# Kernel optimization log

Measured on AMD Instinct MI355X. Metric: run time of the kernel, lower is better.

Reference implementation:

```python
import jax, jax.numpy as jnp
import numpy as np

N, F, D, E, L, T = 20000, 512, 256, 200000, 3, 2  # nodes, raw feat, hidden, edges/etype, layers, etypes


def _layernorm(x, g, b, eps=1e-5):
    mu = jnp.mean(x, axis=-1, keepdims=True)
    var = jnp.mean(jnp.square(x - mu), axis=-1, keepdims=True)
    return (x - mu) * jax.lax.rsqrt(var + eps) * g + b


def setup_inputs() -> dict:
    key = jax.random.key(0)
    ks = jax.random.split(key, 12)
    s = 0.02
    return {
        "x": jax.random.normal(ks[0], (N, F), dtype=jnp.float32),
        "src": jax.random.randint(ks[1], (T, E), 0, N, dtype=jnp.int32),
        "dst": jax.random.randint(ks[2], (T, E), 0, N, dtype=jnp.int32),
        # HeteroLinear (single ntype)
        "Wlin": jax.random.normal(ks[3], (D, F), dtype=jnp.float32) * s,
        "blin": jnp.zeros((D,), dtype=jnp.float32),
        # stacked per-layer, per-etype SAGEConv('pool') params
        "Wpool": jax.random.normal(ks[4], (L, T, D, D), dtype=jnp.float32) * s,
        "bpool": jnp.zeros((L, T, D), dtype=jnp.float32),
        "Wself": jax.random.normal(ks[5], (L, T, D, D), dtype=jnp.float32) * s,
        "Wneigh": jax.random.normal(ks[6], (L, T, D, D), dtype=jnp.float32) * s,
        "bconv": jnp.zeros((L, T, D), dtype=jnp.float32),
        "gamma": jnp.ones((L, T, D), dtype=jnp.float32),
        "beta": jnp.zeros((L, T, D), dtype=jnp.float32),
    }


def reference(x, src, dst, Wlin, blin, Wpool, bpool, Wself, Wneigh, bconv, gamma, beta):
    n = x.shape[0]
    # HeteroLinear: raw features -> embed
    h = x @ Wlin.T + blin
    for l in range(L):
        out = None
        for t in range(T):  # per edge-type SAGEConv, aggregator='pool'
            hp = jax.nn.relu(h @ Wpool[l, t].T + bpool[l, t])        # fc_pool + relu on src nodes
            m = hp[src[t]]                                            # gather [E, D]
            neigh = jax.ops.segment_max(m, dst[t], num_segments=n)    # max-pool reduce
            neigh = jnp.where(jnp.isneginf(neigh), 0.0, neigh)        # zero-in-degree -> 0 (DGL)
            rst = h @ Wself[l, t].T + neigh @ Wneigh[l, t].T + bconv[l, t]
            if l < L - 1:
                rst = jax.nn.relu(rst)                                # activation before norm
            rst = _layernorm(rst, gamma[l, t], beta[l, t])
            out = rst if out is None else out + rst                   # HeteroGraphConv 'sum'
        h = out
    return h
```

## Files before the change

### kernel.cpp

```cpp
#include <hip/hip_runtime.h>

#define N_NODES 20000
#define F_IN    512
#define D_H     256
#define E_EDGES 200000
#define L_LAYERS 3
#define T_ETYPES 2

typedef __attribute__((ext_vector_type(8))) short bf16x8;
typedef __attribute__((ext_vector_type(4))) float f32x4;

__device__ __forceinline__ unsigned short f2b(float f) {
    unsigned int u = __float_as_uint(f);
    u = (u + 0x7FFFu + ((u >> 16) & 1u)) >> 16;
    return (unsigned short)u;
}
__device__ __forceinline__ unsigned int pack2(float a, float b) {
    return (unsigned int)f2b(a) | ((unsigned int)f2b(b) << 16);
}

__device__ __forceinline__ void gload16(const unsigned short* g, unsigned short* l)
{
    __builtin_amdgcn_global_load_lds(
        (const __attribute__((address_space(1))) void*)g,
        (__attribute__((address_space(3))) void*)l, 16, 0, 0);
}

__device__ __forceinline__ void shuf_one(const float* s, unsigned short* d,
                                         int NO, int K, int i)
{
    const int matsz = NO * K;
    const int mat = i / matsz;
    const int rem = i - mat * matsz;
    const int n = rem / K;
    const int k = rem - n * K;
    const int dst = mat * matsz + ((n >> 7) * (K >> 5) + (k >> 5)) * 4096
                  + (((n >> 4) & 7) << 9) + (((k >> 3) & 3) << 7)
                  + ((n & 15) << 3) + (k & 7);
    d[dst] = f2b(s[i]);
}

__global__ __launch_bounds__(256) void shufw_kernel(
    const float* __restrict__ s0, unsigned short* __restrict__ d0, int NO0, int K0, int n0,
    const float* __restrict__ s1, unsigned short* __restrict__ d1, int NO1, int K1, int n1,
    const float* __restrict__ s2, unsigned short* __restrict__ d2, int NO2, int K2, int n2,
    const float* __restrict__ s3, unsigned short* __restrict__ d3, int NO3, int K3, int n3)
{
    int i = blockIdx.x * 256 + threadIdx.x;
    if (i < n0) { shuf_one(s0, d0, NO0, K0, i); return; }
    if ((i -= n0) < n1) { shuf_one(s1, d1, NO1, K1, i); return; }
    if ((i -= n1) < n2) { shuf_one(s2, d2, NO2, K2, i); return; }
    if ((i -= n2) < n3) { shuf_one(s3, d3, NO3, K3, i); return; }
}

__global__ __launch_bounds__(256) void cvt_bf16_kernel(
    const float* __restrict__ in, unsigned short* __restrict__ out, int n8)
{
    const int i = blockIdx.x * 256 + threadIdx.x;
    if (i < n8) {
        const float4 a = ((const float4*)in)[i * 2];
        const float4 b = ((const float4*)in)[i * 2 + 1];
        uint4 u;
        u.x = pack2(a.x, a.y); u.y = pack2(a.z, a.w);
        u.z = pack2(b.x, b.y); u.w = pack2(b.z, b.w);
        ((uint4*)out)[i] = u;
    }
}

template <int NSTEPS>
__global__ __launch_bounds__(256) void gemm_lds(
    const unsigned short* __restrict__ A,
    const unsigned short* __restrict__ Wf,
    const float* __restrict__ bias, unsigned short* __restrict__ Cout,
    int M, int ldc, int relu)
{
    __shared__ __align__(16) unsigned short As[2][4096];
    __shared__ __align__(16) unsigned short Bs[2][4096];
    const int K = NSTEPS * 32;
    const int tid = threadIdx.x, lane = tid & 63, w = tid >> 6;
    const int wm = w >> 1, wn = w & 1;
    const int bm = blockIdx.y * 128, bn = blockIdx.x * 128;
    const unsigned short* slab0 = Wf + (((size_t)blockIdx.x * NSTEPS) << 12);

    size_t aoff[2];
#pragma unroll
    for (int q = 0; q < 2; ++q) {
        const int c = q * 256 + tid;
        const int mi = c >> 6, ww = c & 63, r = ww & 15, kq = ww >> 4;
        const int rg = min(bm + mi * 16 + r, M - 1);
        aoff[q] = (size_t)rg * K + kq * 8;
    }

    f32x4 acc[4][4] = {};

#define GL_STAGE(S, BUF) do { \
    _Pragma("unroll") \
    for (int q_ = 0; q_ < 2; ++q_) { \
        gload16(A + aoff[q_] + (S) * 32, &As[BUF][(q_ * 256 + w * 64) * 8]); \
        gload16(slab0 + (((size_t)(S)) << 12) + (size_t)(q_ * 256 + tid) * 8, \
                &Bs[BUF][(q_ * 256 + w * 64) * 8]); \
    } \
} while (0)

    GL_STAGE(0, 0);
#pragma unroll
    for (int s = 0; s < NSTEPS; ++s) {
        __syncthreads();
        if (s + 1 < NSTEPS) GL_STAGE(s + 1, (s + 1) & 1);
        const int buf = s & 1;
        bf16x8 a[4], b[4];
#pragma unroll
        for (int mi = 0; mi < 4; ++mi)
            a[mi] = *(const bf16x8*)((const char*)As[buf] + ((wm * 4 + mi) << 10) + lane * 16);
#pragma unroll
        for (int j = 0; j < 4; ++j)
            b[j] = *(const bf16x8*)((const char*)Bs[buf] + ((wn * 4 + j) << 10) + lane * 16);
#pragma unroll
        for (int mi = 0; mi < 4; ++mi)
#pragma unroll
            for (int j = 0; j < 4; ++j)
                acc[mi][j] = __builtin_amdgcn_mfma_f32_16x16x32_bf16(a[mi], b[j], acc[mi][j], 0, 0, 0);
    }
#undef GL_STAGE

    const int cbase = bn + wn * 64 + (lane & 15);
    const int rb = bm + wm * 64 + ((lane >> 4) << 2);
#pragma unroll
    for (int j = 0; j < 4; ++j) {
        const float bj = bias[cbase + j * 16];
#pragma unroll
        for (int mi = 0; mi < 4; ++mi)
#pragma unroll
            for (int r = 0; r < 4; ++r) {
                const int row = rb + mi * 16 + r;
                if (row < M) {
                    float v = acc[mi][j][r] + bj;
                    if (relu) v = fmaxf(v, 0.f);
                    Cout[(size_t)row * ldc + cbase + j * 16] = f2b(v);
                }
            }
    }
}

template <int RELU>
__global__ __launch_bounds__(256) void tail_gemm(
    const unsigned short* __restrict__ h,
    const unsigned short* __restrict__ neigh,
    const unsigned short* __restrict__ Ws,
    const unsigned short* __restrict__ Wn,
    const float* __restrict__ bias,
    float* __restrict__ R)
{
    __shared__ __align__(16) unsigned short As[2][4096];
    __shared__ __align__(16) unsigned short Bs[2][4096];
    const int tid = threadIdx.x, lane = tid & 63, w = tid >> 6;
    const int wm = w >> 1, wn = w & 1;
    const int bm = blockIdx.y * 128;
    const int cs = blockIdx.x;
    const int e  = cs >> 1;
    const unsigned short* Bself  = Ws + (size_t)e * 65536 + (cs & 1) * 32768;
    const unsigned short* Bneigh = Wn + (size_t)e * 65536 + (cs & 1) * 32768;

    size_t aoffH[2], aoffN[2];
#pragma unroll
    for (int q = 0; q < 2; ++q) {
        const int c = q * 256 + tid;
        const int mi = c >> 6, ww = c & 63, r = ww & 15, kq = ww >> 4;
        const int rg = min(bm + mi * 16 + r, N_NODES - 1);
        aoffH[q] = (size_t)rg * 256 + kq * 8;
        aoffN[q] = (size_t)rg * 512 + e * 256 + kq * 8;
    }

    f32x4 acc[4][4] = {};

#define TG_STAGE(S, BUF) do { \
    _Pragma("unroll") \
    for (int q_ = 0; q_ < 2; ++q_) { \
        const unsigned short* as_ = ((S) < 8) ? (h + aoffH[q_] + (S) * 32) \
                                              : (neigh + aoffN[q_] + ((S) - 8) * 32); \
        gload16(as_, &As[BUF][(q_ * 256 + w * 64) * 8]); \
        const unsigned short* bs_ = (((S) < 8) ? (Bself + (S) * 4096) \
                                               : (Bneigh + ((S) - 8) * 4096)) \
                                    + (size_t)(q_ * 256 + tid) * 8; \
        gload16(bs_, &Bs[BUF][(q_ * 256 + w * 64) * 8]); \
    } \
} while (0)

    TG_STAGE(0, 0);
#pragma unroll
    for (int s = 0; s < 16; ++s) {
        __syncthreads();
        if (s + 1 < 16) TG_STAGE(s + 1, (s + 1) & 1);
        const int buf = s & 1;
        bf16x8 a[4], b[4];
#pragma unroll
        for (int mi = 0; mi < 4; ++mi)
            a[mi] = *(const bf16x8*)((const char*)As[buf] + ((wm * 4 + mi) << 10) + lane * 16);
#pragma unroll
        for (int j = 0; j < 4; ++j)
            b[j] = *(const bf16x8*)((const char*)Bs[buf] + ((wn * 4 + j) << 10) + lane * 16);
#pragma unroll
        for (int mi = 0; mi < 4; ++mi)
#pragma unroll
            for (int j = 0; j < 4; ++j)
                acc[mi][j] = __builtin_amdgcn_mfma_f32_16x16x32_bf16(a[mi], b[j], acc[mi][j], 0, 0, 0);
    }
#undef TG_STAGE

    const int cbase = cs * 128 + wn * 64 + (lane & 15);
    const int rb = bm + wm * 64 + ((lane >> 4) << 2);
#pragma unroll
    for (int j = 0; j < 4; ++j) {
        const float bj = bias[cbase + j * 16];
#pragma unroll
        for (int mi = 0; mi < 4; ++mi)
#pragma unroll
            for (int r = 0; r < 4; ++r) {
                const int row = rb + mi * 16 + r;
                if (row < N_NODES) {
                    float v = acc[mi][j][r] + bj;
                    if (RELU) v = fmaxf(v, 0.f);
                    R[(size_t)row * 512 + cbase + j * 16] = v;
                }
            }
    }
}

template <int LAST>
__global__ __launch_bounds__(256) void ln_sum_kernel(
    const float* __restrict__ R,
    const float* __restrict__ gamma,
    const float* __restrict__ beta,
    void* __restrict__ outp)
{
    const int row  = blockIdx.x * 4 + (threadIdx.x >> 6);
    const int lane = threadIdx.x & 63;
    const float4 v0 = ((const float4*)R)[(size_t)row * 128 + lane];
    const float4 v1 = ((const float4*)R)[(size_t)row * 128 + 64 + lane];
    float s0 = v0.x + v0.y + v0.z + v0.w;
    float q0 = v0.x * v0.x + v0.y * v0.y + v0.z * v0.z + v0.w * v0.w;
    float s1 = v1.x + v1.y + v1.z + v1.w;
    float q1 = v1.x * v1.x + v1.y * v1.y + v1.z * v1.z + v1.w * v1.w;
#pragma unroll
    for (int o = 1; o < 64; o <<= 1) {
        s0 += __shfl_xor(s0, o); q0 += __shfl_xor(q0, o);
        s1 += __shfl_xor(s1, o); q1 += __shfl_xor(q1, o);
    }
    const float m0 = s0 * (1.f / 256.f), m1 = s1 * (1.f / 256.f);
    const float i0 = rsqrtf(q0 * (1.f / 256.f) - m0 * m0 + 1e-5f);
    const float i1 = rsqrtf(q1 * (1.f / 256.f) - m1 * m1 + 1e-5f);
    const float4 g0 = ((const float4*)gamma)[lane];
    const float4 b0 = ((const float4*)beta)[lane];
    const float4 g1 = ((const float4*)(gamma + 256))[lane];
    const float4 b1 = ((const float4*)(beta + 256))[lane];
    const float o0 = (v0.x - m0) * i0 * g0.x + b0.x + (v1.x - m1) * i1 * g1.x + b1.x;
    const float o1 = (v0.y - m0) * i0 * g0.y + b0.y + (v1.y - m1) * i1 * g1.y + b1.y;
    const float o2 = (v0.z - m0) * i0 * g0.z + b0.z + (v1.z - m1) * i1 * g1.z + b1.z;
    const float o3 = (v0.w - m0) * i0 * g0.w + b0.w + (v1.w - m1) * i1 * g1.w + b1.w;
    if (LAST) {
        ((float4*)outp)[(size_t)row * 64 + lane] = make_float4(o0, o1, o2, o3);
    } else {
        ushort4 u;
        u.x = f2b(o0); u.y = f2b(o1); u.z = f2b(o2); u.w = f2b(o3);
        ((ushort4*)outp)[(size_t)row * 64 + lane] = u;
    }
}

__global__ __launch_bounds__(256) void count_deg_kernel(
    const int* __restrict__ dst, int* __restrict__ cnt, int E2)
{
    int e = blockIdx.x * 256 + threadIdx.x;
    if (e < E2) {
        const int base = (e >= E_EDGES) ? N_NODES : 0;
        atomicAdd(&cnt[base + dst[e]], 1);
    }
}

__global__ __launch_bounds__(256) void scanA_kernel(
    const int* __restrict__ cnt, int* __restrict__ incl, int* __restrict__ bsum, int n)
{
    __shared__ int tmp[256];
    const int tid = threadIdx.x;
    const int i = blockIdx.x * 256 + tid;
    const int v = (i < n) ? cnt[i] : 0;
    tmp[tid] = v;
    __syncthreads();
#pragma unroll
    for (int o = 1; o < 256; o <<= 1) {
        const int t = (tid >= o) ? tmp[tid - o] : 0;
        __syncthreads();
        tmp[tid] += t;
        __syncthreads();
    }
    if (i < n) incl[i] = tmp[tid];
    if (tid == 255) bsum[blockIdx.x] = tmp[255];
}

__global__ __launch_bounds__(256) void scanB_kernel(int* __restrict__ bsum, int nb)
{
    __shared__ int tmp[256];
    const int tid = threadIdx.x;
    const int v = (tid < nb) ? bsum[tid] : 0;
    tmp[tid] = v;
    __syncthreads();
#pragma unroll
    for (int o = 1; o < 256; o <<= 1) {
        const int t = (tid >= o) ? tmp[tid - o] : 0;
        __syncthreads();
        tmp[tid] += t;
        __syncthreads();
    }
    if (tid < nb) bsum[tid] = tmp[tid] - v;
}

__global__ __launch_bounds__(256) void scanC_kernel(
    const int* __restrict__ cnt, const int* __restrict__ incl,
    const int* __restrict__ bsum, int* __restrict__ off, int* __restrict__ cursor, int n)
{
    const int i = blockIdx.x * 256 + threadIdx.x;
    if (i < n) {
        const int e = incl[i] + bsum[blockIdx.x];
        off[i + 1] = e;
        cursor[i] = e - cnt[i];
    }
    if (i == 0) off[0] = 0;
}

__global__ __launch_bounds__(256) void fill_csr_kernel(
    const int* __restrict__ src, const int* __restrict__ dst,
    int* __restrict__ cursor, int* __restrict__ esrc, int E2)
{
    int e = blockIdx.x * 256 + threadIdx.x;
    if (e < E2) {
        const int base = (e >= E_EDGES) ? N_NODES : 0;
        const int pos = atomicAdd(&cursor[base + dst[e]], 1);
        esrc[pos] = src[e];
    }
}

__device__ __forceinline__ ushort4 umax4(ushort4 a, ushort4 b)
{
    a.x = a.x > b.x ? a.x : b.x;
    a.y = a.y > b.y ? a.y : b.y;
    a.z = a.z > b.z ? a.z : b.z;
    a.w = a.w > b.w ? a.w : b.w;
    return a;
}

__global__ __launch_bounds__(256) void seg_max_kernel(
    const unsigned short* __restrict__ hp, const int* __restrict__ off,
    const int* __restrict__ esrc, unsigned short* __restrict__ neigh)
{
    const int g = blockIdx.x * 4 + (threadIdx.x >> 6);
    if (g >= 2 * N_NODES) return;
    const int t = (g >= N_NODES) ? 1 : 0;
    const int node = g - t * N_NODES;
    const int lane = threadIdx.x & 63;
    const int co = t * D_H + lane * 4;
    const int e0 = off[g], e1 = off[g + 1];
    ushort4 acc = make_ushort4(0, 0, 0, 0);
    int e = e0;
    for (; e + 4 <= e1; e += 4) {
        const int s0 = esrc[e + 0], s1 = esrc[e + 1];
        const int s2 = esrc[e + 2], s3 = esrc[e + 3];
        const ushort4 v0 = *(const ushort4*)(hp + (size_t)s0 * 512 + co);
        const ushort4 v1 = *(const ushort4*)(hp + (size_t)s1 * 512 + co);
        const ushort4 v2 = *(const ushort4*)(hp + (size_t)s2 * 512 + co);
        const ushort4 v3 = *(const ushort4*)(hp + (size_t)s3 * 512 + co);
        acc = umax4(umax4(umax4(acc, v0), umax4(v1, v2)), v3);
    }
    for (; e < e1; ++e)
        acc = umax4(acc, *(const ushort4*)(hp + (size_t)esrc[e] * 512 + co));
    *(ushort4*)(neigh + (size_t)node * 512 + co) = acc;
}

extern "C" void kernel_launch(void* const* d_in, const int* in_sizes, int n_in,
                              void* d_out, int out_size, void* d_ws, size_t ws_size,
                              hipStream_t stream)
{
    const float* x      = (const float*)d_in[0];
    const int*   src    = (const int*)d_in[1];
    const int*   dst    = (const int*)d_in[2];
    const float* Wlin   = (const float*)d_in[3];
    const float* blin   = (const float*)d_in[4];
    const float* Wpool  = (const float*)d_in[5];
    const float* bpool  = (const float*)d_in[6];
    const float* Wself  = (const float*)d_in[7];
    const float* Wneigh = (const float*)d_in[8];
    const float* bconv  = (const float*)d_in[9];
    const float* gamma  = (const float*)d_in[10];
    const float* beta   = (const float*)d_in[11];

    const size_t NB = (size_t)N_NODES * D_H;
    char* p = (char*)d_ws;
    unsigned short* hp_b    = (unsigned short*)p; p += NB * 2 * T_ETYPES;
    unsigned short* neigh_b = (unsigned short*)p; p += NB * 2 * T_ETYPES;
    unsigned short* h_a     = (unsigned short*)p; p += NB * 2;
    unsigned short* h_b     = (unsigned short*)p; p += NB * 2;
    unsigned short* xb      = (unsigned short*)p; p += (size_t)N_NODES * F_IN * 2;
    float*          Rbuf    = (float*)p;          p += (size_t)N_NODES * 512 * 4;
    unsigned short* wlin_f  = (unsigned short*)p; p += (size_t)D_H * F_IN * 2;
    const size_t WSZ = (size_t)L_LAYERS * T_ETYPES * D_H * D_H;
    unsigned short* wpool_f = (unsigned short*)p; p += WSZ * 2;
    unsigned short* wself_f = (unsigned short*)p; p += WSZ * 2;
    unsigned short* wneigh_f= (unsigned short*)p; p += WSZ * 2;
    int* ip = (int*)p;
    const int NT = T_ETYPES * N_NODES;
    int* cnt    = ip; ip += NT;
    int* incl   = ip; ip += NT;
    int* off    = ip; ip += NT + 1;
    int* cursor = ip; ip += NT;
    int* esrc   = ip; ip += T_ETYPES * E_EDGES;
    int* bsum   = ip; ip += 256;

    const dim3 blk(256);
    const int E2 = T_ETYPES * E_EDGES;
    const dim3 e2grid((E2 + 255) / 256);
    const int nScanBlk = (NT + 255) / 256;

    {
        const int nlin = D_H * F_IN;
        const int nw   = (int)WSZ;
        const int tot  = nlin + 3 * nw;
        shufw_kernel<<<dim3((tot + 255) / 256), blk, 0, stream>>>(
            Wlin, wlin_f, D_H, F_IN, nlin,
            Wpool, wpool_f, T_ETYPES * D_H, D_H, nw,
            Wself, wself_f, D_H, D_H, nw,
            Wneigh, wneigh_f, D_H, D_H, nw);
    }

    cvt_bf16_kernel<<<dim3((N_NODES * F_IN / 8 + 255) / 256), blk, 0, stream>>>(
        x, xb, N_NODES * F_IN / 8);

    hipMemsetAsync(cnt, 0, (size_t)NT * sizeof(int), stream);
    count_deg_kernel<<<e2grid, blk, 0, stream>>>(dst, cnt, E2);
    scanA_kernel<<<dim3(nScanBlk), blk, 0, stream>>>(cnt, incl, bsum, NT);
    scanB_kernel<<<dim3(1), blk, 0, stream>>>(bsum, nScanBlk);
    scanC_kernel<<<dim3(nScanBlk), blk, 0, stream>>>(cnt, incl, bsum, off, cursor, NT);
    fill_csr_kernel<<<e2grid, blk, 0, stream>>>(src, dst, cursor, esrc, E2);

    const int MB = (N_NODES + 127) / 128;

    gemm_lds<16><<<dim3(2, MB), blk, 0, stream>>>(
        xb, wlin_f, blin, h_a, N_NODES, D_H, 0);

    unsigned short* h = h_a;
    unsigned short* hn = h_b;
    const dim3 sgrid((2 * N_NODES + 3) / 4);
    const dim3 lngrid(N_NODES / 4);
    for (int l = 0; l < L_LAYERS; ++l) {
        gemm_lds<8><<<dim3(4, MB), blk, 0, stream>>>(
            h, wpool_f + (size_t)l * T_ETYPES * D_H * D_H,
            bpool + (size_t)l * T_ETYPES * D_H, hp_b, N_NODES, T_ETYPES * D_H, 1);
        seg_max_kernel<<<sgrid, blk, 0, stream>>>(hp_b, off, esrc, neigh_b);
        const size_t wlo = (size_t)l * T_ETYPES * D_H * D_H;
        const size_t blo = (size_t)l * T_ETYPES * D_H;
        if (l < L_LAYERS - 1) {
            tail_gemm<1><<<dim3(4, MB), blk, 0, stream>>>(
                h, neigh_b, wself_f + wlo, wneigh_f + wlo, bconv + blo, Rbuf);
            ln_sum_kernel<0><<<lngrid, blk, 0, stream>>>(
                Rbuf, gamma + blo, beta + blo, hn);
        } else {
            tail_gemm<0><<<dim3(4, MB), blk, 0, stream>>>(
                h, neigh_b, wself_f + wlo, wneigh_f + wlo, bconv + blo, Rbuf);
            ln_sum_kernel<1><<<lngrid, blk, 0, stream>>>(
                Rbuf, gamma + blo, beta + blo, d_out);
        }
        unsigned short* tmp = h; h = hn; hn = tmp;
    }
}
```

Baseline: 459.2 us.

## Triple-buffer GEMM LDS pipeline and fuse weight shuffle with input conversion

Both GEMM kernels move from a double-buffered LDS pipeline with __syncthreads to a three-stage ring. Loads are issued two steps ahead, and each step waits with an explicit s_waitcnt vmcnt plus a raw barrier, so global-to-LDS latency is hidden better. Bias loads are hoisted ahead of the main loop. The weight reshuffle now handles 8 elements per thread with vector loads and stores, and it is merged with the x bf16 conversion into one launch. The cost is 50% more LDS per block, which may lower occupancy, and the hand-tuned vmcnt count is a correctness risk if the per-stage load count changes.

Result: faster. 410.2 us (-10.7%).

```diff
diff --git a/kernel.cpp b/kernel.cpp
--- a/kernel.cpp
+++ b/kernel.cpp
@@ -26,45 +26,52 @@
         (__attribute__((address_space(3))) void*)l, 16, 0, 0);
 }
 
-__device__ __forceinline__ void shuf_one(const float* s, unsigned short* d,
-                                         int NO, int K, int i)
-{
-    const int matsz = NO * K;
-    const int mat = i / matsz;
-    const int rem = i - mat * matsz;
-    const int n = rem / K;
-    const int k = rem - n * K;
-    const int dst = mat * matsz + ((n >> 7) * (K >> 5) + (k >> 5)) * 4096
-                  + (((n >> 4) & 7) << 9) + (((k >> 3) & 3) << 7)
-                  + ((n & 15) << 3) + (k & 7);
-    d[dst] = f2b(s[i]);
-}
-
-__global__ __launch_bounds__(256) void shufw_kernel(
-    const float* __restrict__ s0, unsigned short* __restrict__ d0, int NO0, int K0, int n0,
-    const float* __restrict__ s1, unsigned short* __restrict__ d1, int NO1, int K1, int n1,
-    const float* __restrict__ s2, unsigned short* __restrict__ d2, int NO2, int K2, int n2,
-    const float* __restrict__ s3, unsigned short* __restrict__ d3, int NO3, int K3, int n3)
+__device__ __forceinline__ void shufg8(const float* __restrict__ s,
+                                       unsigned short* __restrict__ d,
+                                       int NO, int K, int o8)
+{
+    const int matsz8 = (NO * K) >> 3;
+    const int mat = o8 / matsz8;
+    const int rem = o8 - mat * matsz8;
+    const int dst = rem << 3;
+    const int slab = dst >> 12;
+    const int w = dst & 4095;
+    const int spr = K >> 5;
+    const int slab_n = slab / spr, slab_k = slab - slab_n * spr;
+    const int nl = (((w >> 9) & 7) << 4) + ((w >> 3) & 15);
+    const int kk = ((w >> 7) & 3) << 3;
+    const size_t soff = (size_t)mat * NO * K + (size_t)(slab_n * 128 + nl) * K
+                      + slab_k * 32 + kk;
+    const float4 a = *(const float4*)(s + soff);
+    const float4 b = *(const float4*)(s + soff + 4);
+    uint4 u;
+    u.x = pack2(a.x, a.y); u.y = pack2(a.z, a.w);
+    u.z = pack2(b.x, b.y); u.w = pack2(b.z, b.w);
+    *(uint4*)(d + (size_t)mat * NO * K + dst) = u;
+}
+
+__global__ __launch_bounds__(256) void prep_kernel(
+    const float* __restrict__ x,  unsigned short* __restrict__ xb, int nx8,
+    const float* __restrict__ s0, unsigned short* __restrict__ d0, int NO0, int K0, int n08,
+    const float* __restrict__ s1, unsigned short* __restrict__ d1, int NO1, int K1, int n18,
+    const float* __restrict__ s2, unsigned short* __restrict__ d2, int NO2, int K2, int n28,
+    const float* __restrict__ s3, unsigned short* __restrict__ d3, int NO3, int K3, int n38)
 {
     int i = blockIdx.x * 256 + threadIdx.x;
-    if (i < n0) { shuf_one(s0, d0, NO0, K0, i); return; }
-    if ((i -= n0) < n1) { shuf_one(s1, d1, NO1, K1, i); return; }
-    if ((i -= n1) < n2) { shuf_one(s2, d2, NO2, K2, i); return; }
-    if ((i -= n2) < n3) { shuf_one(s3, d3, NO3, K3, i); return; }
-}
-
-__global__ __launch_bounds__(256) void cvt_bf16_kernel(
-    const float* __restrict__ in, unsigned short* __restrict__ out, int n8)
-{
-    const int i = blockIdx.x * 256 + threadIdx.x;
-    if (i < n8) {
-        const float4 a = ((const float4*)in)[i * 2];
-        const float4 b = ((const float4*)in)[i * 2 + 1];
+    if (i < nx8) {
+        const float4 a = ((const float4*)x)[i * 2];
+        const float4 b = ((const float4*)x)[i * 2 + 1];
         uint4 u;
         u.x = pack2(a.x, a.y); u.y = pack2(a.z, a.w);
         u.z = pack2(b.x, b.y); u.w = pack2(b.z, b.w);
-        ((uint4*)out)[i] = u;
-    }
+        ((uint4*)xb)[i] = u;
+        return;
+    }
+    i -= nx8;
+    if (i < n08) { shufg8(s0, d0, NO0, K0, i); return; }
+    if ((i -= n08) < n18) { shufg8(s1, d1, NO1, K1, i); return; }
+    if ((i -= n18) < n28) { shufg8(s2, d2, NO2, K2, i); return; }
+    if ((i -= n28) < n38) { shufg8(s3, d3, NO3, K3, i); return; }
 }
 
 template <int NSTEPS>
@@ -74,8 +81,8 @@
     const float* __restrict__ bias, unsigned short* __restrict__ Cout,
     int M, int ldc, int relu)
 {
-    __shared__ __align__(16) unsigned short As[2][4096];
-    __shared__ __align__(16) unsigned short Bs[2][4096];
+    __shared__ __align__(16) unsigned short As[3][4096];
+    __shared__ __align__(16) unsigned short Bs[3][4096];
     const int K = NSTEPS * 32;
     const int tid = threadIdx.x, lane = tid & 63, w = tid >> 6;
     const int wm = w >> 1, wn = w & 1;
@@ -90,6 +97,12 @@
         const int rg = min(bm + mi * 16 + r, M - 1);
         aoff[q] = (size_t)rg * K + kq * 8;
     }
+
+    const int cbase = bn + wn * 64 + (lane & 15);
+    float bj[4];
+#pragma unroll
+    for (int j = 0; j < 4; ++j) bj[j] = bias[cbase + j * 16];
+    asm volatile("" ::: "memory");
 
     f32x4 acc[4][4] = {};
 
@@ -103,11 +116,15 @@
 } while (0)
 
     GL_STAGE(0, 0);
+    GL_STAGE(1, 1);
 #pragma unroll
     for (int s = 0; s < NSTEPS; ++s) {
-        __syncthreads();
-        if (s + 1 < NSTEPS) GL_STAGE(s + 1, (s + 1) & 1);
-        const int buf = s & 1;
+        if (s + 1 < NSTEPS) asm volatile("s_waitcnt vmcnt(4)" ::: "memory");
+        else                asm volatile("s_waitcnt vmcnt(0)" ::: "memory");
+        __builtin_amdgcn_s_barrier();
+        asm volatile("" ::: "memory");
+        if (s + 2 < NSTEPS) GL_STAGE(s + 2, (s + 2) % 3);
+        const int buf = s % 3;
         bf16x8 a[4], b[4];
 #pragma unroll
         for (int mi = 0; mi < 4; ++mi)
@@ -123,18 +140,16 @@
     }
 #undef GL_STAGE
 
-    const int cbase = bn + wn * 64 + (lane & 15);
     const int rb = bm + wm * 64 + ((lane >> 4) << 2);
 #pragma unroll
     for (int j = 0; j < 4; ++j) {
-        const float bj = bias[cbase + j * 16];
 #pragma unroll
         for (int mi = 0; mi < 4; ++mi)
 #pragma unroll
             for (int r = 0; r < 4; ++r) {
                 const int row = rb + mi * 16 + r;
                 if (row < M) {
-                    float v = acc[mi][j][r] + bj;
+                    float v = acc[mi][j][r] + bj[j];
                     if (relu) v = fmaxf(v, 0.f);
                     Cout[(size_t)row * ldc + cbase + j * 16] = f2b(v);
                 }
@@ -151,8 +166,8 @@
     const float* __restrict__ bias,
     float* __restrict__ R)
 {
-    __shared__ __align__(16) unsigned short As[2][4096];
-    __shared__ __align__(16) unsigned short Bs[2][4096];
+    __shared__ __align__(16) unsigned short As[3][4096];
+    __shared__ __align__(16) unsigned short Bs[3][4096];
     const int tid = threadIdx.x, lane = tid & 63, w = tid >> 6;
     const int wm = w >> 1, wn = w & 1;
     const int bm = blockIdx.y * 128;
@@ -170,6 +185,12 @@
         aoffH[q] = (size_t)rg * 256 + kq * 8;
         aoffN[q] = (size_t)rg * 512 + e * 256 + kq * 8;
     }
+
+    const int cbase = cs * 128 + wn * 64 + (lane & 15);
+    float bj[4];
+#pragma unroll
+    for (int j = 0; j < 4; ++j) bj[j] = bias[cbase + j * 16];
+    asm volatile("" ::: "memory");
 
     f32x4 acc[4][4] = {};
 
@@ -187,11 +208,15 @@
 } while (0)
 
     TG_STAGE(0, 0);
+    TG_STAGE(1, 1);
 #pragma unroll
     for (int s = 0; s < 16; ++s) {
-        __syncthreads();
-        if (s + 1 < 16) TG_STAGE(s + 1, (s + 1) & 1);
-        const int buf = s & 1;
+        if (s + 1 < 16) asm volatile("s_waitcnt vmcnt(4)" ::: "memory");
+        else            asm volatile("s_waitcnt vmcnt(0)" ::: "memory");
+        __builtin_amdgcn_s_barrier();
+        asm volatile("" ::: "memory");
+        if (s + 2 < 16) TG_STAGE(s + 2, (s + 2) % 3);
+        const int buf = s % 3;
         bf16x8 a[4], b[4];
 #pragma unroll
         for (int mi = 0; mi < 4; ++mi)
@@ -207,18 +232,16 @@
     }
 #undef TG_STAGE
 
-    const int cbase = cs * 128 + wn * 64 + (lane & 15);
     const int rb = bm + wm * 64 + ((lane >> 4) << 2);
 #pragma unroll
     for (int j = 0; j < 4; ++j) {
-        const float bj = bias[cbase + j * 16];
 #pragma unroll
         for (int mi = 0; mi < 4; ++mi)
 #pragma unroll
             for (int r = 0; r < 4; ++r) {
                 const int row = rb + mi * 16 + r;
                 if (row < N_NODES) {
-                    float v = acc[mi][j][r] + bj;
+                    float v = acc[mi][j][r] + bj[j];
                     if (RELU) v = fmaxf(v, 0.f);
                     R[(size_t)row * 512 + cbase + j * 16] = v;
                 }
@@ -419,18 +442,17 @@
     const int nScanBlk = (NT + 255) / 256;
 
     {
-        const int nlin = D_H * F_IN;
-        const int nw   = (int)WSZ;
-        const int tot  = nlin + 3 * nw;
-        shufw_kernel<<<dim3((tot + 255) / 256), blk, 0, stream>>>(
-            Wlin, wlin_f, D_H, F_IN, nlin,
-            Wpool, wpool_f, T_ETYPES * D_H, D_H, nw,
-            Wself, wself_f, D_H, D_H, nw,
-            Wneigh, wneigh_f, D_H, D_H, nw);
-    }
-
-    cvt_bf16_kernel<<<dim3((N_NODES * F_IN / 8 + 255) / 256), blk, 0, stream>>>(
-        x, xb, N_NODES * F_IN / 8);
+        const int nx8  = N_NODES * F_IN / 8;
+        const int nl8  = D_H * F_IN / 8;
+        const int nw8  = (int)(WSZ / 8);
+        const int tot  = nx8 + nl8 + 3 * nw8;
+        prep_kernel<<<dim3((tot + 255) / 256), blk, 0, stream>>>(
+            x, xb, nx8,
+            Wlin, wlin_f, D_H, F_IN, nl8,
+            Wpool, wpool_f, T_ETYPES * D_H, D_H, nw8,
+            Wself, wself_f, D_H, D_H, nw8,
+            Wneigh, wneigh_f, D_H, D_H, nw8);
+    }
 
     hipMemsetAsync(cnt, 0, (size_t)NT * sizeof(int), stream);
     count_deg_kernel<<<e2grid, blk, 0, stream>>>(dst, cnt, E2);
```
